# Kernel optimization log

Measured on AMD Instinct MI355X. Metric: run time of the kernel, lower is better.

Reference implementation:

```python
import jax, jax.numpy as jnp
import numpy as np

N_NODES = 10000
N_EDGES = 160000
N_MAP = 50000
F_DIM = 128
N_RBF = 20
CUTOFF = 5.0
NUM_CONV = 3
EPS = 1e-15


def _w(k, shape):
    # simple fan-in scaled init for Dense weights (stored as (L, in, out))
    return jax.random.normal(k, shape, jnp.float32) * (1.0 / float(np.sqrt(shape[-2])))


def setup_inputs() -> dict:
    key = jax.random.key(0)
    ks = jax.random.split(key, 16)
    cg_xyz = jax.random.normal(ks[0], (N_NODES, 3), jnp.float32)
    src = jax.random.randint(ks[1], (N_EDGES,), 0, N_NODES)
    off = jax.random.randint(ks[2], (N_EDGES,), 1, N_NODES)
    dst = (src + off) % N_NODES  # directed neighbor list, no self-edges
    CG_nbr_list = jnp.stack([src, dst], axis=-1)
    mapping = jax.random.randint(ks[3], (N_MAP,), 0, N_NODES)
    H = jax.random.normal(ks[4], (N_NODES, F_DIM), jnp.float32)
    L, F = NUM_CONV, F_DIM
    params = dict(
        msg_W1=_w(ks[5], (L, 2 * F, 2 * F)), msg_b1=jnp.zeros((L, 2 * F), jnp.float32),
        msg_W2=_w(ks[6], (L, 2 * F, 5 * F)), msg_b2=jnp.zeros((L, 5 * F), jnp.float32),
        dist_W=_w(ks[7], (L, N_RBF, 5 * F)), dist_b=jnp.zeros((L, 5 * F), jnp.float32),
        upd_U=_w(ks[8], (L, F, F)), upd_V=_w(ks[9], (L, F, F)),
        upd_W1=_w(ks[10], (L, 2 * F, F)), upd_b1=jnp.zeros((L, F), jnp.float32),
        upd_W2=_w(ks[11], (L, F, 3 * F)), upd_b2=jnp.zeros((L, 3 * F), jnp.float32),
    )
    return dict(cg_xyz=cg_xyz, CG_nbr_list=CG_nbr_list, mapping=mapping, H=H, **params)


def reference(cg_xyz, CG_nbr_list, mapping, H,
              msg_W1, msg_b1, msg_W2, msg_b2, dist_W, dist_b,
              upd_U, upd_V, upd_W1, upd_b1, upd_W2, upd_b2):
    act = jax.nn.silu  # 'swish'
    N = H.shape[0]
    src = CG_nbr_list[:, 0]
    dst = CG_nbr_list[:, 1]
    # edge geometry (preprocess_r)
    r_ij = cg_xyz[dst] - cg_xyz[src]                 # (E, 3)
    dist = jnp.sqrt(jnp.sum(r_ij ** 2, axis=-1))     # (E,)
    unit = r_ij / dist[:, None]                      # (E, 3)
    # PaiNN radial basis sin(n*pi*d/cutoff)/d and cosine cutoff envelope
    n = jnp.arange(1, N_RBF + 1, dtype=cg_xyz.dtype)
    rbf = jnp.sin(n[None, :] * (jnp.pi / CUTOFF) * dist[:, None]) / dist[:, None]  # (E, n_rbf)
    env = jnp.where(dist < CUTOFF, 0.5 * (jnp.cos(jnp.pi * dist / CUTOFF) + 1.0), 0.0)  # (E,)
    # state init (breaksym=False -> Sbar zeros)
    V = jnp.zeros((N, F_DIM, 3), H.dtype)
    Sbar = jnp.zeros_like(H)
    Vbar = jnp.zeros_like(V)
    for l in range(NUM_CONV):
        # ---- EquiMessagePsuedo ----
        s_cat = jnp.concatenate([H, Sbar], axis=-1)                          # (N, 2F)
        phi = act(s_cat @ msg_W1[l] + msg_b1[l]) @ msg_W2[l] + msg_b2[l]     # (N, 5F)
        w_s = (rbf @ dist_W[l] + dist_b[l]) * env[:, None]                   # (E, 5F)
        inv = (phi[dst] * w_s).reshape(-1, 5, F_DIM)                         # (E, 5, F)
        gate_v = inv[:, 0, :][..., None]   # gates v_j
        ds = inv[:, 1, :]
        dir_coef = inv[:, 2, :][..., None]  # scales unit vector (shared)
        dsbar = inv[:, 3, :]
        gate_vbar = inv[:, 4, :][..., None]  # gates vbar_j
        unit_add = dir_coef * unit[:, None, :]                               # (E, F, 3)
        dv_ij = unit_add + gate_v * V[dst]
        dvbar_ij = unit_add + gate_vbar * Vbar[dst]
        H = H + jax.ops.segment_sum(ds, src, num_segments=N)
        Sbar = Sbar + jax.ops.segment_sum(dsbar, src, num_segments=N)
        V = V + jax.ops.segment_sum(dv_ij, src, num_segments=N)
        Vbar = Vbar + jax.ops.segment_sum(dvbar_ij, src, num_segments=N)
        # ---- UpdateBlock (standard PaiNN update) ----
        u_v = jnp.einsum('nfd,fg->ngd', V, upd_U[l])                          # (N, F, 3)
        v_v = jnp.einsum('nfd,fg->ngd', V, upd_V[l])                          # (N, F, 3)
        v_norm = jnp.sqrt(jnp.sum(v_v ** 2, axis=-1) + EPS)                   # (N, F)
        s_stack = jnp.concatenate([H, v_norm], axis=-1)                       # (N, 2F)
        a = act(s_stack @ upd_W1[l] + upd_b1[l]) @ upd_W2[l] + upd_b2[l]      # (N, 3F)
        a = a.reshape(-1, 3, F_DIM)
        dV_u = u_v * a[:, 0, :][..., None]
        dH_u = a[:, 1, :] * jnp.sum(u_v * v_v, axis=-1) + a[:, 2, :]
        H = H + dH_u
        V = V + dV_u
    return H, V
```

## Files before the change

### kernel.cpp

```cpp
#include <hip/hip_runtime.h>
#include <math.h>

#define NN 10000
#define NE 160000
#define FDIM 128
#define NRBF 20
#define PI_F 3.14159265358979323846f
#define LDP 40

typedef short bf16x8 __attribute__((ext_vector_type(8)));
typedef float f32x4 __attribute__((ext_vector_type(4)));

__device__ __forceinline__ unsigned short f2bf_rne(float v) {
    unsigned int u = __float_as_uint(v);
    u += 0x7FFF + ((u >> 16) & 1);
    return (unsigned short)(u >> 16);
}
__device__ __forceinline__ float bf2f(unsigned short b) {
    return __uint_as_float(((unsigned int)b) << 16);
}

__global__ void edge_count_kernel(const int* __restrict__ nbr, int* __restrict__ counts)
{
    int e = blockIdx.x * blockDim.x + threadIdx.x;
    if (e >= NE) return;
    atomicAdd(&counts[nbr[2 * e]], 1);
}

__global__ void scan_kernel(const int* __restrict__ counts, int* __restrict__ offsets)
{
    __shared__ int sd[1024];
    __shared__ int carry;
    if (threadIdx.x == 0) carry = 0;
    __syncthreads();
    for (int base = 0; base < NN; base += 1024) {
        int i = base + threadIdx.x;
        int v = (i < NN) ? counts[i] : 0;
        sd[threadIdx.x] = v;
        __syncthreads();
        for (int off = 1; off < 1024; off <<= 1) {
            int t = (threadIdx.x >= off) ? sd[threadIdx.x - off] : 0;
            __syncthreads();
            sd[threadIdx.x] += t;
            __syncthreads();
        }
        if (i < NN) offsets[i] = carry + sd[threadIdx.x] - v;
        __syncthreads();
        if (threadIdx.x == 0) carry += sd[1023];
        __syncthreads();
    }
    if (threadIdx.x == 0) offsets[NN] = carry;
}

__global__ void edge_geom_fill_kernel(const float* __restrict__ xyz, const int* __restrict__ nbr,
                                      const int* __restrict__ offsets, int* __restrict__ cnt2,
                                      int* __restrict__ dstP, float4* __restrict__ ueP,
                                      float* __restrict__ rbfP)
{
    int e = blockIdx.x * blockDim.x + threadIdx.x;
    if (e >= NE) return;
    int s = nbr[2 * e], d = nbr[2 * e + 1];
    float dx = xyz[3 * d + 0] - xyz[3 * s + 0];
    float dy = xyz[3 * d + 1] - xyz[3 * s + 1];
    float dz = xyz[3 * d + 2] - xyz[3 * s + 2];
    float dist = sqrtf(dx * dx + dy * dy + dz * dz);
    float inv = 1.0f / dist;
    int p = offsets[s] + atomicAdd(&cnt2[s], 1);
    dstP[p] = d;
    const float c = PI_F / 5.0f;
    float env = (dist < 5.0f) ? 0.5f * (cosf(c * dist) + 1.0f) : 0.0f;
    ueP[p] = make_float4(dx * inv, dy * inv, dz * inv, env);
#pragma unroll
    for (int k = 0; k < NRBF; k++)
        rbfP[NRBF * p + k] = sinf((float)(k + 1) * c * dist) * inv;
}

__global__ void build_uvcat_kernel(const float* __restrict__ updU,
                                   const float* __restrict__ updV,
                                   float* __restrict__ UVcat)
{
    int idx = blockIdx.x * blockDim.x + threadIdx.x;
    if (idx >= 3 * 128 * 256) return;
    int l = idx / (128 * 256);
    int rem = idx % (128 * 256);
    int k = rem >> 8, j = rem & 255;
    UVcat[idx] = (j < 128) ? updU[(l * 128 + k) * 128 + j]
                           : updV[(l * 128 + k) * 128 + (j - 128)];
}

template <int ACT, int CAT>
__global__ __launch_bounds__(256) void gemm3_kernel(
    const float* __restrict__ A0, const float* __restrict__ A1,
    const float* __restrict__ W, const float* __restrict__ bias,
    float* __restrict__ C, int M, int K, int N)
{
    __shared__ __align__(16) unsigned short Ah[64 * LDP];
    __shared__ __align__(16) unsigned short Al[64 * LDP];
    __shared__ __align__(16) unsigned short Bh[64 * LDP];
    __shared__ __align__(16) unsigned short Bl[64 * LDP];

    int tid = threadIdx.x;
    int row0 = blockIdx.y * 64, col0 = blockIdx.x * 64;
    int lane = tid & 63, wave = tid >> 6;
    int mb = (wave & 1) * 32, nb = (wave >> 1) * 32;
    int lm = lane & 15, quad = lane >> 4;

    f32x4 acc[2][2] = {};

    int ra = tid >> 2, kq = tid & 3;
    int kr = tid >> 3, nq = tid & 7;

    for (int k0 = 0; k0 < K; k0 += 32) {
        {
            int ar = row0 + ra;
            float4 a0 = make_float4(0.f, 0.f, 0.f, 0.f);
            float4 a1 = make_float4(0.f, 0.f, 0.f, 0.f);
            if (ar < M) {
                const float* Ab;
                if (CAT) Ab = (k0 < 128) ? A0 + (size_t)ar * 128 + k0
                                         : A1 + (size_t)ar * 128 + (k0 - 128);
                else     Ab = A0 + (size_t)ar * K + k0;
                a0 = *(const float4*)(Ab + kq * 4);
                a1 = *(const float4*)(Ab + kq * 4 + 16);
            }
            float v0[4] = {a0.x, a0.y, a0.z, a0.w};
            float v1[4] = {a1.x, a1.y, a1.z, a1.w};
            ushort4 h0, l0, h1, l1;
            unsigned short* hp0 = (unsigned short*)&h0;
            unsigned short* lp0 = (unsigned short*)&l0;
            unsigned short* hp1 = (unsigned short*)&h1;
            unsigned short* lp1 = (unsigned short*)&l1;
#pragma unroll
            for (int i = 0; i < 4; i++) {
                unsigned short h = f2bf_rne(v0[i]);
                hp0[i] = h; lp0[i] = f2bf_rne(v0[i] - bf2f(h));
                unsigned short g = f2bf_rne(v1[i]);
                hp1[i] = g; lp1[i] = f2bf_rne(v1[i] - bf2f(g));
            }
            *(ushort4*)&Ah[ra * LDP + kq * 4]      = h0;
            *(ushort4*)&Al[ra * LDP + kq * 4]      = l0;
            *(ushort4*)&Ah[ra * LDP + kq * 4 + 16] = h1;
            *(ushort4*)&Al[ra * LDP + kq * 4 + 16] = l1;
        }
        {
            const float* Wb = &W[(size_t)(k0 + kr) * N + col0];
            float4 b0 = *(const float4*)(Wb + nq * 4);
            float4 b1 = *(const float4*)(Wb + nq * 4 + 32);
            float v0[4] = {b0.x, b0.y, b0.z, b0.w};
            float v1[4] = {b1.x, b1.y, b1.z, b1.w};
#pragma unroll
            for (int i = 0; i < 4; i++) {
                int n = nq * 4 + i;
                unsigned short h = f2bf_rne(v0[i]);
                Bh[n * LDP + kr] = h;
                Bl[n * LDP + kr] = f2bf_rne(v0[i] - bf2f(h));
                int n2 = n + 32;
                unsigned short g = f2bf_rne(v1[i]);
                Bh[n2 * LDP + kr] = g;
                Bl[n2 * LDP + kr] = f2bf_rne(v1[i] - bf2f(g));
            }
        }
        __syncthreads();
        bf16x8 fah[2], fal[2], fbh[2], fbl[2];
#pragma unroll
        for (int mt = 0; mt < 2; mt++) {
            int r = mb + mt * 16 + lm;
            fah[mt] = *(const bf16x8*)&Ah[r * LDP + quad * 8];
            fal[mt] = *(const bf16x8*)&Al[r * LDP + quad * 8];
        }
#pragma unroll
        for (int nt = 0; nt < 2; nt++) {
            int n = nb + nt * 16 + lm;
            fbh[nt] = *(const bf16x8*)&Bh[n * LDP + quad * 8];
            fbl[nt] = *(const bf16x8*)&Bl[n * LDP + quad * 8];
        }
#pragma unroll
        for (int mt = 0; mt < 2; mt++)
#pragma unroll
            for (int nt = 0; nt < 2; nt++) {
                acc[mt][nt] = __builtin_amdgcn_mfma_f32_16x16x32_bf16(
                    fah[mt], fbh[nt], acc[mt][nt], 0, 0, 0);
                acc[mt][nt] = __builtin_amdgcn_mfma_f32_16x16x32_bf16(
                    fah[mt], fbl[nt], acc[mt][nt], 0, 0, 0);
                acc[mt][nt] = __builtin_amdgcn_mfma_f32_16x16x32_bf16(
                    fal[mt], fbh[nt], acc[mt][nt], 0, 0, 0);
            }
        __syncthreads();
    }
#pragma unroll
    for (int mt = 0; mt < 2; mt++)
#pragma unroll
        for (int nt = 0; nt < 2; nt++) {
            int c = col0 + nb + nt * 16 + lm;
            float bv = bias ? bias[c] : 0.f;
#pragma unroll
            for (int reg = 0; reg < 4; reg++) {
                int r = row0 + mb + mt * 16 + quad * 4 + reg;
                if (r >= M) continue;
                float v = acc[mt][nt][reg] + bv;
                if (ACT) v = v / (1.0f + expf(-v));
                C[(size_t)r * N + c] = v;
            }
        }
}

__global__ __launch_bounds__(256, 4) void gather_kernel(
    const int* __restrict__ offsets, const int* __restrict__ dstP,
    const float4* __restrict__ ueP, const float* __restrict__ rbfP,
    const float* __restrict__ phi,
    const float* __restrict__ distW, const float* __restrict__ distb,
    const float* __restrict__ Vold, const float* __restrict__ Vbold,
    float* __restrict__ H, float* __restrict__ Sbar,
    float* __restrict__ Vnew, float* __restrict__ Vbnew)
{
    int n = blockIdx.x;
    int t = threadIdx.x;
    int half = t >> 7;
    int f = t & 127;
    int po = half * 256;

    float wv[60];
#pragma unroll
    for (int k = 0; k < NRBF; k++)
#pragma unroll
        for (int c = 0; c < 3; c++)
            wv[k * 3 + c] = distW[k * 640 + po + c * 128 + f];
#pragma unroll
    for (int i = 0; i < 60; i++) asm volatile("" : "+v"(wv[i]));

    float bA = distb[po + f], bB = distb[po + 128 + f], bC = distb[po + 256 + f];

    const float* Vsel = half ? Vbold : Vold;

    float sacc = 0.f, acc0 = 0.f, acc1 = 0.f, acc2 = 0.f;
    int e0 = offsets[n], e1 = offsets[n + 1];
    for (int p = e0; p < e1; ++p) {
        int d = dstP[p];
        float4 ue = ueP[p];
        float r[NRBF];
#pragma unroll
        for (int q = 0; q < NRBF / 4; q++) {
            float4 rv = *(const float4*)&rbfP[NRBF * p + 4 * q];
            r[4 * q + 0] = rv.x; r[4 * q + 1] = rv.y;
            r[4 * q + 2] = rv.z; r[4 * q + 3] = rv.w;
        }
        float wA = bA, wB = bB, wC = bC;
#pragma unroll
        for (int k = 0; k < NRBF; k++) {
            float rk = r[k];
            wA += rk * wv[k * 3 + 0];
            wB += rk * wv[k * 3 + 1];
            wC += rk * wv[k * 3 + 2];
        }
        float ev = ue.w;
        const float* ph = phi + (size_t)d * 640 + po;
        float iA = ph[f] * wA * ev;
        float iB = ph[128 + f] * wB * ev;
        float iC = ph[256 + f] * wC * ev;
        float dir  = half ? iA : iC;
        float gate = half ? iC : iA;
        sacc += iB;
        const float* vd = Vsel + (size_t)d * 384;
        acc0 += dir * ue.x + gate * vd[f];
        acc1 += dir * ue.y + gate * vd[128 + f];
        acc2 += dir * ue.z + gate * vd[256 + f];
    }
    if (half == 0) H[n * 128 + f] += sacc;
    else           Sbar[n * 128 + f] += sacc;
    const float* vo = Vsel + (size_t)n * 384;
    float* vn = (half ? Vbnew : Vnew) + (size_t)n * 384;
    vn[f]       = vo[f]       + acc0;
    vn[128 + f] = vo[128 + f] + acc1;
    vn[256 + f] = vo[256 + f] + acc2;
}

__global__ void norm_kernel(const float* __restrict__ uv2,
                            float* __restrict__ vnorm, float* __restrict__ dotb)
{
    int idx = blockIdx.x * blockDim.x + threadIdx.x;
    if (idx >= NN * 128) return;
    int n = idx >> 7, g = idx & 127;
    const float* base = uv2 + (size_t)n * 768;
    float u0 = base[g],       u1 = base[256 + g], u2 = base[512 + g];
    float v0 = base[128 + g], v1 = base[384 + g], v2 = base[640 + g];
    dotb[idx] = u0 * v0 + u1 * v1 + u2 * v2;
    vnorm[idx] = sqrtf(v0 * v0 + v1 * v1 + v2 * v2 + 1e-15f);
}

template <int LAST>
__global__ void final_update_kernel(const float* __restrict__ a,
                                    const float* __restrict__ dotb,
                                    const float* __restrict__ uv2,
                                    float* __restrict__ H,
                                    float* __restrict__ Vplanar,
                                    float* __restrict__ Vout)
{
    int idx = blockIdx.x * blockDim.x + threadIdx.x;
    if (idx >= NN * 128) return;
    int n = idx >> 7, g = idx & 127;
    float a0 = a[n * 384 + g];
    float a1 = a[n * 384 + 128 + g];
    float a2 = a[n * 384 + 256 + g];
    H[idx] += a1 * dotb[idx] + a2;
    float* vp = Vplanar + (size_t)n * 384;
    const float* ub = uv2 + (size_t)n * 768;
    float v0 = vp[g]       + a0 * ub[g];
    float v1 = vp[128 + g] + a0 * ub[256 + g];
    float v2 = vp[256 + g] + a0 * ub[512 + g];
    if (LAST) {
        float* o = Vout + (size_t)n * 384 + g * 3;
        o[0] = v0; o[1] = v1; o[2] = v2;
    } else {
        vp[g] = v0; vp[128 + g] = v1; vp[256 + g] = v2;
    }
}

extern "C" void kernel_launch(void* const* d_in, const int* in_sizes, int n_in,
                              void* d_out, int out_size, void* d_ws, size_t ws_size,
                              hipStream_t stream)
{
    const float* xyz    = (const float*)d_in[0];
    const int*   nbr    = (const int*)d_in[1];
    const float* H_in   = (const float*)d_in[3];
    const float* msgW1  = (const float*)d_in[4];
    const float* msgb1  = (const float*)d_in[5];
    const float* msgW2  = (const float*)d_in[6];
    const float* msgb2  = (const float*)d_in[7];
    const float* distW  = (const float*)d_in[8];
    const float* distb  = (const float*)d_in[9];
    const float* updU   = (const float*)d_in[10];
    const float* updV   = (const float*)d_in[11];
    const float* updW1  = (const float*)d_in[12];
    const float* updb1  = (const float*)d_in[13];
    const float* updW2  = (const float*)d_in[14];
    const float* updb2  = (const float*)d_in[15];

    float* out  = (float*)d_out;
    float* H    = out;
    float* Vout = out + NN * 128;

    float* f = (float*)d_ws;
    float* Va   = f; f += NN * 384;
    float* Vb   = f; f += NN * 384;
    float* Vba  = f; f += NN * 384;
    float* Vbb  = f; f += NN * 384;
    float* Sbar = f; f += NN * 128;
    float* X1   = f; f += NN * 256;
    float* phi  = f; f += NN * 640;
    float* uv2  = f; f += NN * 768;
    float* UVcat = f; f += 3 * 128 * 256;
    float4* ueP = (float4*)f; f += NE * 4;
    float* rbfP  = f; f += NE * NRBF;
    int* ip = (int*)f;
    int* counts  = ip; ip += NN;
    int* offsets = ip; ip += NN + 1;
    int* cnt2    = ip; ip += NN;
    int* dstP    = ip; ip += NE;
    float* vnorm = phi;
    float* dotb  = phi + NN * 128;
    float* abuf  = phi + NN * 256;

    hipMemsetAsync(counts, 0, NN * sizeof(int), stream);
    hipMemsetAsync(cnt2, 0, NN * sizeof(int), stream);
    hipMemsetAsync(Va, 0, (size_t)NN * 384 * sizeof(float), stream);
    hipMemsetAsync(Vba, 0, (size_t)NN * 384 * sizeof(float), stream);
    hipMemsetAsync(Sbar, 0, (size_t)NN * 128 * sizeof(float), stream);
    hipMemcpyAsync(H, H_in, (size_t)NN * 128 * sizeof(float),
                   hipMemcpyDeviceToDevice, stream);

    edge_count_kernel<<<(NE + 255) / 256, 256, 0, stream>>>(nbr, counts);
    scan_kernel<<<1, 1024, 0, stream>>>(counts, offsets);
    edge_geom_fill_kernel<<<(NE + 255) / 256, 256, 0, stream>>>(xyz, nbr, offsets, cnt2,
                                                                dstP, ueP, rbfP);
    build_uvcat_kernel<<<(3 * 128 * 256 + 255) / 256, 256, 0, stream>>>(updU, updV, UVcat);

    for (int l = 0; l < 3; ++l) {
        const float* W1 = msgW1 + (size_t)l * 256 * 256;
        const float* b1 = msgb1 + (size_t)l * 256;
        const float* W2 = msgW2 + (size_t)l * 256 * 640;
        const float* b2 = msgb2 + (size_t)l * 640;
        const float* dW = distW + (size_t)l * NRBF * 640;
        const float* db = distb + (size_t)l * 640;
        const float* UVl = UVcat + (size_t)l * 128 * 256;
        const float* uW1 = updW1 + (size_t)l * 256 * 128;
        const float* ub1 = updb1 + (size_t)l * 128;
        const float* uW2 = updW2 + (size_t)l * 128 * 384;
        const float* ub2 = updb2 + (size_t)l * 384;

        float *Vold, *Vnew, *Vbold, *Vbnew;
        if (l == 0)      { Vold = Va; Vnew = Vb; Vbold = Vba; Vbnew = Vbb; }
        else if (l == 1) { Vold = Vb; Vnew = Va; Vbold = Vbb; Vbnew = Vba; }
        else             { Vold = Va; Vnew = Vb; Vbold = Vba; Vbnew = Vbb; }

        {
            dim3 g(256 / 64, (NN + 63) / 64);
            gemm3_kernel<1, 1><<<g, 256, 0, stream>>>(H, Sbar, W1, b1, X1, NN, 256, 256);
        }
        {
            dim3 g(640 / 64, (NN + 63) / 64);
            gemm3_kernel<0, 0><<<g, 256, 0, stream>>>(X1, nullptr, W2, b2, phi, NN, 256, 640);
        }

        gather_kernel<<<NN, 256, 0, stream>>>(offsets, dstP, ueP, rbfP,
                                              phi, dW, db, Vold, Vbold,
                                              H, Sbar, Vnew, Vbnew);

        {
            dim3 g(256 / 64, (3 * NN + 63) / 64);
            gemm3_kernel<0, 0><<<g, 256, 0, stream>>>(Vnew, nullptr, UVl, nullptr,
                                                      uv2, 3 * NN, 128, 256);
        }
        norm_kernel<<<(NN * 128 + 255) / 256, 256, 0, stream>>>(uv2, vnorm, dotb);

        {
            dim3 g(128 / 64, (NN + 63) / 64);
            gemm3_kernel<1, 1><<<g, 256, 0, stream>>>(H, vnorm, uW1, ub1, X1, NN, 256, 128);
        }
        {
            dim3 g(384 / 64, (NN + 63) / 64);
            gemm3_kernel<0, 0><<<g, 256, 0, stream>>>(X1, nullptr, uW2, ub2, abuf, NN, 128, 384);
        }

        if (l < 2)
            final_update_kernel<0><<<(NN * 128 + 255) / 256, 256, 0, stream>>>(
                abuf, dotb, uv2, H, Vnew, nullptr);
        else
            final_update_kernel<1><<<(NN * 128 + 255) / 256, 256, 0, stream>>>(
                abuf, dotb, uv2, H, Vnew, Vout);
    }
}
```

Baseline: 932.3 us.

## Pre-split weights and intermediates into bf16 hi/lo, specialize first-layer gather

```diff
diff --git a/kernel.cpp b/kernel.cpp
--- a/kernel.cpp
+++ b/kernel.cpp
@@ -10,6 +10,7 @@
 
 typedef short bf16x8 __attribute__((ext_vector_type(8)));
 typedef float f32x4 __attribute__((ext_vector_type(4)));
+typedef float v2f __attribute__((ext_vector_type(2)));
 
 __device__ __forceinline__ unsigned short f2bf_rne(float v) {
     unsigned int u = __float_as_uint(v);
@@ -75,24 +76,43 @@
         rbfP[NRBF * p + k] = sinf((float)(k + 1) * c * dist) * inv;
 }
 
+__global__ void split_kernel(const float* __restrict__ src,
+                             unsigned short* __restrict__ h,
+                             unsigned short* __restrict__ l, int n)
+{
+    int idx = blockIdx.x * blockDim.x + threadIdx.x;
+    if (idx >= n) return;
+    float v = src[idx];
+    unsigned short hh = f2bf_rne(v);
+    h[idx] = hh;
+    l[idx] = f2bf_rne(v - bf2f(hh));
+}
+
 __global__ void build_uvcat_kernel(const float* __restrict__ updU,
                                    const float* __restrict__ updV,
-                                   float* __restrict__ UVcat)
+                                   unsigned short* __restrict__ h,
+                                   unsigned short* __restrict__ l)
 {
     int idx = blockIdx.x * blockDim.x + threadIdx.x;
     if (idx >= 3 * 128 * 256) return;
-    int l = idx / (128 * 256);
+    int ly = idx / (128 * 256);
     int rem = idx % (128 * 256);
     int k = rem >> 8, j = rem & 255;
-    UVcat[idx] = (j < 128) ? updU[(l * 128 + k) * 128 + j]
-                           : updV[(l * 128 + k) * 128 + (j - 128)];
-}
-
-template <int ACT, int CAT>
-__global__ __launch_bounds__(256) void gemm3_kernel(
-    const float* __restrict__ A0, const float* __restrict__ A1,
-    const float* __restrict__ W, const float* __restrict__ bias,
-    float* __restrict__ C, int M, int K, int N)
+    float v = (j < 128) ? updU[(ly * 128 + k) * 128 + j]
+                        : updV[(ly * 128 + k) * 128 + (j - 128)];
+    unsigned short hh = f2bf_rne(v);
+    h[idx] = hh;
+    l[idx] = f2bf_rne(v - bf2f(hh));
+}
+
+template <int ACT, int CAT, int ASPLIT, int OSPLIT>
+__global__ __launch_bounds__(256) void gemm4_kernel(
+    const float* __restrict__ Af, const float* __restrict__ A1,
+    const unsigned short* __restrict__ Agh, const unsigned short* __restrict__ Agl,
+    const unsigned short* __restrict__ Wh_g, const unsigned short* __restrict__ Wl_g,
+    const float* __restrict__ bias,
+    float* __restrict__ C, unsigned short* __restrict__ Ch, unsigned short* __restrict__ Cl,
+    int M, int K, int N)
 {
     __shared__ __align__(16) unsigned short Ah[64 * LDP];
     __shared__ __align__(16) unsigned short Al[64 * LDP];
@@ -113,51 +133,70 @@
     for (int k0 = 0; k0 < K; k0 += 32) {
         {
             int ar = row0 + ra;
-            float4 a0 = make_float4(0.f, 0.f, 0.f, 0.f);
-            float4 a1 = make_float4(0.f, 0.f, 0.f, 0.f);
-            if (ar < M) {
-                const float* Ab;
-                if (CAT) Ab = (k0 < 128) ? A0 + (size_t)ar * 128 + k0
-                                         : A1 + (size_t)ar * 128 + (k0 - 128);
-                else     Ab = A0 + (size_t)ar * K + k0;
-                a0 = *(const float4*)(Ab + kq * 4);
-                a1 = *(const float4*)(Ab + kq * 4 + 16);
+            if (ASPLIT) {
+                ushort4 h0 = {0, 0, 0, 0}, h1 = {0, 0, 0, 0};
+                ushort4 l0 = {0, 0, 0, 0}, l1 = {0, 0, 0, 0};
+                if (ar < M) {
+                    const unsigned short* bh = Agh + (size_t)ar * K + k0;
+                    const unsigned short* bl = Agl + (size_t)ar * K + k0;
+                    h0 = *(const ushort4*)(bh + kq * 4);
+                    h1 = *(const ushort4*)(bh + kq * 4 + 16);
+                    l0 = *(const ushort4*)(bl + kq * 4);
+                    l1 = *(const ushort4*)(bl + kq * 4 + 16);
+                }
+                *(ushort4*)&Ah[ra * LDP + kq * 4]      = h0;
+                *(ushort4*)&Al[ra * LDP + kq * 4]      = l0;
+                *(ushort4*)&Ah[ra * LDP + kq * 4 + 16] = h1;
+                *(ushort4*)&Al[ra * LDP + kq * 4 + 16] = l1;
+            } else {
+                float4 a0 = make_float4(0.f, 0.f, 0.f, 0.f);
+                float4 a1 = make_float4(0.f, 0.f, 0.f, 0.f);
+                if (ar < M) {
+                    const float* Ab;
+                    if (CAT) Ab = (k0 < 128) ? Af + (size_t)ar * 128 + k0
+                                             : A1 + (size_t)ar * 128 + (k0 - 128);
+                    else     Ab = Af + (size_t)ar * K + k0;
+                    a0 = *(const float4*)(Ab + kq * 4);
+                    a1 = *(const float4*)(Ab + kq * 4 + 16);
+                }
+                float v0[4] = {a0.x, a0.y, a0.z, a0.w};
+                float v1[4] = {a1.x, a1.y, a1.z, a1.w};
+                ushort4 h0, l0, h1, l1;
+                unsigned short* hp0 = (unsigned short*)&h0;
+                unsigned short* lp0 = (unsigned short*)&l0;
+                unsigned short* hp1 = (unsigned short*)&h1;
+                unsigned short* lp1 = (unsigned short*)&l1;
+#pragma unroll
+                for (int i = 0; i < 4; i++) {
+                    unsigned short h = f2bf_rne(v0[i]);
+                    hp0[i] = h; lp0[i] = f2bf_rne(v0[i] - bf2f(h));
+                    unsigned short g = f2bf_rne(v1[i]);
+                    hp1[i] = g; lp1[i] = f2bf_rne(v1[i] - bf2f(g));
+                }
+                *(ushort4*)&Ah[ra * LDP + kq * 4]      = h0;
+                *(ushort4*)&Al[ra * LDP + kq * 4]      = l0;
+                *(ushort4*)&Ah[ra * LDP + kq * 4 + 16] = h1;
+                *(ushort4*)&Al[ra * LDP + kq * 4 + 16] = l1;
             }
-            float v0[4] = {a0.x, a0.y, a0.z, a0.w};
-            float v1[4] = {a1.x, a1.y, a1.z, a1.w};
-            ushort4 h0, l0, h1, l1;
-            unsigned short* hp0 = (unsigned short*)&h0;
-            unsigned short* lp0 = (unsigned short*)&l0;
-            unsigned short* hp1 = (unsigned short*)&h1;
-            unsigned short* lp1 = (unsigned short*)&l1;
-#pragma unroll
-            for (int i = 0; i < 4; i++) {
-                unsigned short h = f2bf_rne(v0[i]);
-                hp0[i] = h; lp0[i] = f2bf_rne(v0[i] - bf2f(h));
-                unsigned short g = f2bf_rne(v1[i]);
-                hp1[i] = g; lp1[i] = f2bf_rne(v1[i] - bf2f(g));
-            }
-            *(ushort4*)&Ah[ra * LDP + kq * 4]      = h0;
-            *(ushort4*)&Al[ra * LDP + kq * 4]      = l0;
-            *(ushort4*)&Ah[ra * LDP + kq * 4 + 16] = h1;
-            *(ushort4*)&Al[ra * LDP + kq * 4 + 16] = l1;
-        }
-        {
-            const float* Wb = &W[(size_t)(k0 + kr) * N + col0];
-            float4 b0 = *(const float4*)(Wb + nq * 4);
-            float4 b1 = *(const float4*)(Wb + nq * 4 + 32);
-            float v0[4] = {b0.x, b0.y, b0.z, b0.w};
-            float v1[4] = {b1.x, b1.y, b1.z, b1.w};
+        }
+        {
+            const unsigned short* Wbh = Wh_g + (size_t)(k0 + kr) * N + col0;
+            const unsigned short* Wbl = Wl_g + (size_t)(k0 + kr) * N + col0;
+            ushort4 h0 = *(const ushort4*)(Wbh + nq * 4);
+            ushort4 h1 = *(const ushort4*)(Wbh + nq * 4 + 32);
+            ushort4 l0 = *(const ushort4*)(Wbl + nq * 4);
+            ushort4 l1 = *(const ushort4*)(Wbl + nq * 4 + 32);
+            const unsigned short* hp0 = (const unsigned short*)&h0;
+            const unsigned short* hp1 = (const unsigned short*)&h1;
+            const unsigned short* lp0 = (const unsigned short*)&l0;
+            const unsigned short* lp1 = (const unsigned short*)&l1;
 #pragma unroll
             for (int i = 0; i < 4; i++) {
                 int n = nq * 4 + i;
-                unsigned short h = f2bf_rne(v0[i]);
-                Bh[n * LDP + kr] = h;
-                Bl[n * LDP + kr] = f2bf_rne(v0[i] - bf2f(h));
-                int n2 = n + 32;
-                unsigned short g = f2bf_rne(v1[i]);
-                Bh[n2 * LDP + kr] = g;
-                Bl[n2 * LDP + kr] = f2bf_rne(v1[i] - bf2f(g));
+                Bh[n * LDP + kr] = hp0[i];
+                Bl[n * LDP + kr] = lp0[i];
+                Bh[(n + 32) * LDP + kr] = hp1[i];
+                Bl[(n + 32) * LDP + kr] = lp1[i];
             }
         }
         __syncthreads();
@@ -199,11 +238,18 @@
                 if (r >= M) continue;
                 float v = acc[mt][nt][reg] + bv;
                 if (ACT) v = v / (1.0f + expf(-v));
-                C[(size_t)r * N + c] = v;
+                if (OSPLIT) {
+                    unsigned short h = f2bf_rne(v);
+                    Ch[(size_t)r * N + c] = h;
+                    Cl[(size_t)r * N + c] = f2bf_rne(v - bf2f(h));
+                } else {
+                    C[(size_t)r * N + c] = v;
+                }
             }
         }
 }
 
+template <int L0>
 __global__ __launch_bounds__(256, 4) void gather_kernel(
     const int* __restrict__ offsets, const int* __restrict__ dstP,
     const float4* __restrict__ ueP, const float* __restrict__ rbfP,
@@ -219,14 +265,16 @@
     int f = t & 127;
     int po = half * 256;
 
-    float wv[60];
-#pragma unroll
-    for (int k = 0; k < NRBF; k++)
-#pragma unroll
-        for (int c = 0; c < 3; c++)
-            wv[k * 3 + c] = distW[k * 640 + po + c * 128 + f];
-#pragma unroll
-    for (int i = 0; i < 60; i++) asm volatile("" : "+v"(wv[i]));
+    v2f wv2[30];
+#pragma unroll
+    for (int q = 0; q < 10; q++)
+#pragma unroll
+        for (int c = 0; c < 3; c++) {
+            wv2[q * 3 + c].x = distW[(2 * q) * 640 + po + c * 128 + f];
+            wv2[q * 3 + c].y = distW[(2 * q + 1) * 640 + po + c * 128 + f];
+        }
+#pragma unroll
+    for (int i = 0; i < 30; i++) asm volatile("" : "+v"(wv2[i]));
 
     float bA = distb[po + f], bB = distb[po + 128 + f], bC = distb[po + 256 + f];
 
@@ -244,34 +292,47 @@
             r[4 * q + 0] = rv.x; r[4 * q + 1] = rv.y;
             r[4 * q + 2] = rv.z; r[4 * q + 3] = rv.w;
         }
-        float wA = bA, wB = bB, wC = bC;
-#pragma unroll
-        for (int k = 0; k < NRBF; k++) {
-            float rk = r[k];
-            wA += rk * wv[k * 3 + 0];
-            wB += rk * wv[k * 3 + 1];
-            wC += rk * wv[k * 3 + 2];
+        v2f aA = {0.f, 0.f}, aB = {0.f, 0.f}, aC = {0.f, 0.f};
+#pragma unroll
+        for (int q = 0; q < 10; q++) {
+            v2f r2; r2.x = r[2 * q]; r2.y = r[2 * q + 1];
+            aA += r2 * wv2[q * 3 + 0];
+            aB += r2 * wv2[q * 3 + 1];
+            aC += r2 * wv2[q * 3 + 2];
         }
         float ev = ue.w;
+        float wA = (aA.x + aA.y + bA) * ev;
+        float wB = (aB.x + aB.y + bB) * ev;
+        float wC = (aC.x + aC.y + bC) * ev;
         const float* ph = phi + (size_t)d * 640 + po;
-        float iA = ph[f] * wA * ev;
-        float iB = ph[128 + f] * wB * ev;
-        float iC = ph[256 + f] * wC * ev;
-        float dir  = half ? iA : iC;
-        float gate = half ? iC : iA;
+        float iA = ph[f] * wA;
+        float iB = ph[128 + f] * wB;
+        float iC = ph[256 + f] * wC;
+        float dir = half ? iA : iC;
         sacc += iB;
-        const float* vd = Vsel + (size_t)d * 384;
-        acc0 += dir * ue.x + gate * vd[f];
-        acc1 += dir * ue.y + gate * vd[128 + f];
-        acc2 += dir * ue.z + gate * vd[256 + f];
+        if (L0) {
+            acc0 += dir * ue.x;
+            acc1 += dir * ue.y;
+            acc2 += dir * ue.z;
+        } else {
+            float gate = half ? iC : iA;
+            const float* vd = Vsel + (size_t)d * 384;
+            acc0 += dir * ue.x + gate * vd[f];
+            acc1 += dir * ue.y + gate * vd[128 + f];
+            acc2 += dir * ue.z + gate * vd[256 + f];
+        }
     }
     if (half == 0) H[n * 128 + f] += sacc;
     else           Sbar[n * 128 + f] += sacc;
-    const float* vo = Vsel + (size_t)n * 384;
     float* vn = (half ? Vbnew : Vnew) + (size_t)n * 384;
-    vn[f]       = vo[f]       + acc0;
-    vn[128 + f] = vo[128 + f] + acc1;
-    vn[256 + f] = vo[256 + f] + acc2;
+    if (L0) {
+        vn[f] = acc0; vn[128 + f] = acc1; vn[256 + f] = acc2;
+    } else {
+        const float* vo = Vsel + (size_t)n * 384;
+        vn[f]       = vo[f]       + acc0;
+        vn[128 + f] = vo[128 + f] + acc1;
+        vn[256 + f] = vo[256 + f] + acc2;
+    }
 }
 
 __global__ void norm_kernel(const float* __restrict__ uv2,
@@ -345,13 +406,24 @@
     float* Vba  = f; f += NN * 384;
     float* Vbb  = f; f += NN * 384;
     float* Sbar = f; f += NN * 128;
-    float* X1   = f; f += NN * 256;
     float* phi  = f; f += NN * 640;
     float* uv2  = f; f += NN * 768;
-    float* UVcat = f; f += 3 * 128 * 256;
     float4* ueP = (float4*)f; f += NE * 4;
     float* rbfP  = f; f += NE * NRBF;
-    int* ip = (int*)f;
+    unsigned short* us = (unsigned short*)f;
+    unsigned short* X1h = us; us += NN * 256;
+    unsigned short* X1l = us; us += NN * 256;
+    unsigned short* W1h = us; us += 3 * 256 * 256;
+    unsigned short* W1l = us; us += 3 * 256 * 256;
+    unsigned short* W2h = us; us += 3 * 256 * 640;
+    unsigned short* W2l = us; us += 3 * 256 * 640;
+    unsigned short* UVh = us; us += 3 * 128 * 256;
+    unsigned short* UVl = us; us += 3 * 128 * 256;
+    unsigned short* uW1h = us; us += 3 * 256 * 128;
+    unsigned short* uW1l = us; us += 3 * 256 * 128;
+    unsigned short* uW2h = us; us += 3 * 128 * 384;
+    unsigned short* uW2l = us; us += 3 * 128 * 384;
+    int* ip = (int*)(((size_t)us + 15) & ~(size_t)15);
     int* counts  = ip; ip += NN;
     int* offsets = ip; ip += NN + 1;
     int* cnt2    = ip; ip += NN;
@@ -362,8 +434,6 @@
 
     hipMemsetAsync(counts, 0, NN * sizeof(int), stream);
     hipMemsetAsync(cnt2, 0, NN * sizeof(int), stream);
-    hipMemsetAsync(Va, 0, (size_t)NN * 384 * sizeof(float), stream);
-    hipMemsetAsync(Vba, 0, (size_t)NN * 384 * sizeof(float), stream);
     hipMemsetAsync(Sbar, 0, (size_t)NN * 128 * sizeof(float), stream);
     hipMemcpyAsync(H, H_in, (size_t)NN * 128 * sizeof(float),
                    hipMemcpyDeviceToDevice, stream);
@@ -372,20 +442,24 @@
     scan_kernel<<<1, 1024, 0, stream>>>(counts, offsets);
     edge_geom_fill_kernel<<<(NE + 255) / 256, 256, 0, stream>>>(xyz, nbr, offsets, cnt2,
                                                                 dstP, ueP, rbfP);
-    build_uvcat_kernel<<<(3 * 128 * 256 + 255) / 256, 256, 0, stream>>>(updU, updV, UVcat);
+    split_kernel<<<(3 * 256 * 256 + 255) / 256, 256, 0, stream>>>(msgW1, W1h, W1l, 3 * 256 * 256);
+    split_kernel<<<(3 * 256 * 640 + 255) / 256, 256, 0, stream>>>(msgW2, W2h, W2l, 3 * 256 * 640);
+    split_kernel<<<(3 * 256 * 128 + 255) / 256, 256, 0, stream>>>(updW1, uW1h, uW1l, 3 * 256 * 128);
+    split_kernel<<<(3 * 128 * 384 + 255) / 256, 256, 0, stream>>>(updW2, uW2h, uW2l, 3 * 128 * 384);
+    build_uvcat_kernel<<<(3 * 128 * 256 + 255) / 256, 256, 0, stream>>>(updU, updV, UVh, UVl);
 
     for (int l = 0; l < 3; ++l) {
-        const float* W1 = msgW1 + (size_t)l * 256 * 256;
         const float* b1 = msgb1 + (size_t)l * 256;
-        const float* W2 = msgW2 + (size_t)l * 256 * 640;
         const float* b2 = msgb2 + (size_t)l * 640;
         const float* dW = distW + (size_t)l * NRBF * 640;
         const float* db = distb + (size_t)l * 640;
-        const float* UVl = UVcat + (size_t)l * 128 * 256;
-        const float* uW1 = updW1 + (size_t)l * 256 * 128;
         const float* ub1 = updb1 + (size_t)l * 128;
-        const float* uW2 = updW2 + (size_t)l * 128 * 384;
         const float* ub2 = updb2 + (size_t)l * 384;
+        const unsigned short *w1h = W1h + (size_t)l * 256 * 256, *w1l = W1l + (size_t)l * 256 * 256;
+        const unsigned short *w2h = W2h + (size_t)l * 256 * 640, *w2l = W2l + (size_t)l * 256 * 640;
+        const unsigned short *uvh = UVh + (size_t)l * 128 * 256, *uvl = UVl + (size_t)l * 128 * 256;
+        const unsigned short *u1h = uW1h + (size_t)l * 256 * 128, *u1l = uW1l + (size_t)l * 256 * 128;
+        const unsigned short *u2h = uW2h + (size_t)l * 128 * 384, *u2l = uW2l + (size_t)l * 128 * 384;
 
         float *Vold, *Vnew, *Vbold, *Vbnew;
         if (l == 0)      { Vold = Va; Vnew = Vb; Vbold = Vba; Vbnew = Vbb; }
@@ -394,31 +468,45 @@
 
         {
             dim3 g(256 / 64, (NN + 63) / 64);
-            gemm3_kernel<1, 1><<<g, 256, 0, stream>>>(H, Sbar, W1, b1, X1, NN, 256, 256);
+            gemm4_kernel<1, 1, 0, 1><<<g, 256, 0, stream>>>(
+                H, Sbar, nullptr, nullptr, w1h, w1l, b1,
+                nullptr, X1h, X1l, NN, 256, 256);
         }
         {
             dim3 g(640 / 64, (NN + 63) / 64);
-            gemm3_kernel<0, 0><<<g, 256, 0, stream>>>(X1, nullptr, W2, b2, phi, NN, 256, 640);
-        }
-
-        gather_kernel<<<NN, 256, 0, stream>>>(offsets, dstP, ueP, rbfP,
-                                              phi, dW, db, Vold, Vbold,
-                                              H, Sbar, Vnew, Vbnew);
+            gemm4_kernel<0, 0, 1, 0><<<g, 256, 0, stream>>>(
+                nullptr, nullptr, X1h, X1l, w2h, w2l, b2,
+                phi, nullptr, nullptr, NN, 256, 640);
+        }
+
+        if (l == 0)
+            gather_kernel<1><<<NN, 256, 0, stream>>>(offsets, dstP, ueP, rbfP,
+                                                     phi, dW, db, Vold, Vbold,
+                                                     H, Sbar, Vnew, Vbnew);
+        else
+            gather_kernel<0><<<NN, 256, 0, stream>>>(offsets, dstP, ueP, rbfP,
+                                                     phi, dW, db, Vold, Vbold,
+                                                     H, Sbar, Vnew, Vbnew);
 
         {
             dim3 g(256 / 64, (3 * NN + 63) / 64);
-            gemm3_kernel<0, 0><<<g, 256, 0, stream>>>(Vnew, nullptr, UVl, nullptr,
-                                                      uv2, 3 * NN, 128, 256);
+            gemm4_kernel<0, 0, 0, 0><<<g, 256, 0, stream>>>(
+                Vnew, nullptr, nullptr, nullptr, uvh, uvl, nullptr,
+                uv2, nullptr, nullptr, 3 * NN, 128, 256);
         }
         norm_kernel<<<(NN * 128 + 255) / 256, 256, 0, stream>>>(uv2, vnorm, dotb);
 
         {
             dim3 g(128 / 64, (NN + 63) / 64);
-            gemm3_kernel<1, 1><<<g, 256, 0, stream>>>(H, vnorm, uW1, ub1, X1, NN, 256, 128);
+            gemm4_kernel<1, 1, 0, 1><<<g, 256, 0, stream>>>(
+                H, vnorm, nullptr, nullptr, u1h, u1l, ub1,
+                nullptr, X1h, X1l, NN, 256, 128);
         }
         {
             dim3 g(384 / 64, (NN + 63) / 64);
-            gemm3_kernel<0, 0><<<g, 256, 0, stream>>>(X1, nullptr, uW2, ub2, abuf, NN, 128, 384);
+            gemm4_kernel<0, 0, 1, 0><<<g, 256, 0, stream>>>(
+                nullptr, nullptr, X1h, X1l, u2h, u2l, ub2,
+                abuf, nullptr, nullptr, NN, 128, 384);
         }
 
         if (l < 2)
```

After: 900.6 us. 3.4% less time.
